# Kernel tuning notes

Hardware: AMD Instinct MI355X
Metric: run time of the kernel (lower is better)

Reference implementation:

```python
import jax, jax.numpy as jnp
import numpy as np

# CondInst DynamicMaskHead dims (defaults from cfg)
N_IMG, C_IN, H, W = 2, 8, 100, 152
N_INST = 500
CHANNELS = 8
STRIDE = 8  # mask_feat_stride (P3)
WEIGHT_NUMS = [(C_IN + 2) * CHANNELS, CHANNELS * CHANNELS, CHANNELS]  # [80, 64, 8]
BIAS_NUMS = [CHANNELS, CHANNELS, 1]
NUM_PARAMS = sum(WEIGHT_NUMS) + sum(BIAS_NUMS)  # 169


def setup_inputs() -> dict:
    key = jax.random.key(0)
    k1, k2, k3, k4, k5 = jax.random.split(key, 5)
    mask_feats = jax.random.normal(k1, (N_IMG, C_IN, H, W), jnp.float32)
    mask_head_params = jax.random.normal(k2, (N_INST, NUM_PARAMS), jnp.float32) * 0.1
    # instance centers in input-image pixel coords
    instance_locations = jax.random.uniform(k3, (N_INST, 2), jnp.float32) * jnp.array([W * STRIDE, H * STRIDE], jnp.float32)
    # sizes_of_interest gathered per instance fpn level (values in [64, 512])
    soi = jax.random.uniform(k4, (N_INST,), jnp.float32) * 448.0 + 64.0
    im_inds = jax.random.randint(k5, (N_INST,), 0, N_IMG)
    return {"mask_feats": mask_feats, "mask_head_params": mask_head_params,
            "instance_locations": instance_locations, "soi": soi, "im_inds": im_inds}


def compute_locations(h, w, stride):
    # matches adet compute_locations: center of each stride cell
    sx = jnp.arange(w, dtype=jnp.float32) * stride + stride // 2
    sy = jnp.arange(h, dtype=jnp.float32) * stride + stride // 2
    gy, gx = jnp.meshgrid(sy, sx, indexing="ij")
    return jnp.stack([gx.ravel(), gy.ravel()], axis=1)  # [H*W, 2] as (x, y)


def parse_dynamic_params(params):
    # faithful to parse_dynamic_params: split weights then biases along dim 1
    sizes = WEIGHT_NUMS + BIAS_NUMS
    splits = jnp.split(params, np.cumsum(sizes)[:-1].tolist(), axis=1)
    w0 = splits[0].reshape(N_INST, CHANNELS, C_IN + 2)   # layer0: (C_in+2)->channels
    w1 = splits[1].reshape(N_INST, CHANNELS, CHANNELS)   # layer1: channels->channels
    w2 = splits[2].reshape(N_INST, 1, CHANNELS)          # layer2: channels->1
    b0, b1, b2 = splits[3], splits[4], splits[5]
    return (w0, w1, w2), (b0, b1, b2)


def reference(mask_feats, mask_head_params, instance_locations, soi, im_inds):
    locations = compute_locations(H, W, STRIDE)  # [HW, 2]
    # relative coords: [n_inst, HW, 2] -> [n_inst, 2, HW], normalized by soi
    rel = (instance_locations[:, None, :] - locations[None, :, :]) / soi[:, None, None]
    rel = jnp.transpose(rel, (0, 2, 1)).astype(mask_feats.dtype)
    feats = mask_feats[im_inds].reshape(N_INST, C_IN, H * W)
    x = jnp.concatenate([rel, feats], axis=1)  # [n_inst, C_in+2, HW]
    (w0, w1, w2), (b0, b1, b2) = parse_dynamic_params(mask_head_params)
    # grouped 1x1 convs (groups=n_inst) == per-instance GEMM over pixels
    x = jax.nn.relu(jnp.einsum("noi,nip->nop", w0, x) + b0[:, :, None])
    x = jax.nn.relu(jnp.einsum("noi,nip->nop", w1, x) + b1[:, :, None])
    x = jnp.einsum("noi,nip->nop", w2, x) + b2[:, :, None]
    return x.reshape(N_INST, 1, H, W)  # mask_logits
```

## Files before the change

kernel.cpp:

```cpp
#include <hip/hip_runtime.h>

#define HGT 100
#define WID 152
#define HW (HGT * WID)
#define NINST 500
#define CIN 8
#define CH 8
#define NPARAMS 169
#define PPT 2


typedef float v2f __attribute__((ext_vector_type(2)));

static __device__ __forceinline__ v2f vsplat2(float x) { v2f r = {x, x}; return r; }

static __device__ __forceinline__ v2f vfma2(float w, v2f x, v2f c) {
#if __has_builtin(__builtin_elementwise_fma)
    return __builtin_elementwise_fma(vsplat2(w), x, c);
#else
    v2f r; r.x = fmaf(w, x.x, c.x); r.y = fmaf(w, x.y, c.y); return r;
#endif
}

static __device__ __forceinline__ v2f vrelu2(v2f a) {
#if __has_builtin(__builtin_elementwise_max)
    return __builtin_elementwise_max(a, vsplat2(0.0f));
#else
    v2f r; r.x = fmaxf(a.x, 0.f); r.y = fmaxf(a.y, 0.f); return r;
#endif
}

__global__ __launch_bounds__(256, 8) void dyn_mask_head(
    const float* __restrict__ feats,
    const float* __restrict__ params,
    const float* __restrict__ locs,
    const float* __restrict__ soi,
    const int*  __restrict__ im_inds,
    float* __restrict__ out)
{
    const int n  = blockIdx.y;
    const int q  = blockIdx.x * blockDim.x + threadIdx.x;
    const int p0 = q * PPT;
    if (p0 >= HW) return;

    const int   im      = im_inds[n];
    const float lx      = locs[n * 2 + 0];
    const float ly      = locs[n * 2 + 1];
    const float inv_soi = 1.0f / soi[n];
    const float* __restrict__ P = params + n * NPARAMS;

    const int py  = p0 / WID;
    const int px0 = p0 - py * WID;
    const float rely = (ly - (float)(py * 8 + 4)) * inv_soi;

    v2f relx;
    relx.x = (lx - (float)(px0 * 8 + 4))  * inv_soi;
    relx.y = (lx - (float)(px0 * 8 + 12)) * inv_soi;

    v2f f[CIN];
    const float* fb = feats + (size_t)im * CIN * HW + p0;
#pragma unroll
    for (int j = 0; j < CIN; ++j) {
        const float2 v = *reinterpret_cast<const float2*>(fb + (size_t)j * HW);
        v2f t = {v.x, v.y};
        f[j] = t;
    }

    v2f h0[CH];
#pragma unroll
    for (int c = 0; c < CH; ++c) {
        const float s = fmaf(P[c * 10 + 1], rely, P[152 + c]);
        v2f acc = vfma2(P[c * 10 + 0], relx, vsplat2(s));
#pragma unroll
        for (int i = 0; i < CIN; ++i)
            acc = vfma2(P[c * 10 + 2 + i], f[i], acc);
        h0[c] = vrelu2(acc);
    }

    v2f h1[CH];
#pragma unroll
    for (int c = 0; c < CH; ++c) {
        v2f acc = vfma2(P[80 + c * 8], h0[0], vsplat2(P[160 + c]));
#pragma unroll
        for (int i = 1; i < CH; ++i)
            acc = vfma2(P[80 + c * 8 + i], h0[i], acc);
        h1[c] = vrelu2(acc);
    }

    v2f o = vfma2(P[144], h1[0], vsplat2(P[168]));
#pragma unroll
    for (int i = 1; i < CH; ++i)
        o = vfma2(P[144 + i], h1[i], o);

    float2 ov; ov.x = o.x; ov.y = o.y;
    *reinterpret_cast<float2*>(out + (size_t)n * HW + p0) = ov;
}

extern "C" void kernel_launch(void* const* d_in, const int* in_sizes, int n_in,
                              void* d_out, int out_size, void* d_ws, size_t ws_size,
                              hipStream_t stream) {
    const float* feats   = (const float*)d_in[0];
    const float* params  = (const float*)d_in[1];
    const float* locs    = (const float*)d_in[2];
    const float* soi     = (const float*)d_in[3];
    const int*   im_inds = (const int*)d_in[4];
    float*       out     = (float*)d_out;

    const int pairs_per_inst = HW / PPT;
    dim3 block(256);
    dim3 grid((pairs_per_inst + block.x - 1) / block.x, NINST);
    dyn_mask_head<<<grid, block, 0, stream>>>(feats, params, locs, soi, im_inds, out);
}
```

Baseline: 35.14 us.

## Rewrite mask head as fp16 MFMA over image-sorted instance quads

Replaces the per-pixel scalar FMA kernel with three kernels. The first sorts instances by image into groups of four, the second prepacks each group's dynamic weights into fp16 MFMA fragments (folding the relative coordinates into an affine hi/lo split), and the third runs 32x32x16 MFMAs per 32-pixel tile across 14 quads per wavefront. It aims to cut the FP32 ALU work and reuse each feature load across many instances. In exchange it adds two extra launches and uses fp16 for weights and activations, which reduces precision.

```diff
diff --git a/kernel.cpp b/kernel.cpp
--- a/kernel.cpp
+++ b/kernel.cpp
@@ -1,99 +1,275 @@
 #include <hip/hip_runtime.h>
+#include <stdint.h>
 
 #define HGT 100
 #define WID 152
 #define HW (HGT * WID)
 #define NINST 500
-#define CIN 8
-#define CH 8
 #define NPARAMS 169
-#define PPT 2
-
-
-typedef float v2f __attribute__((ext_vector_type(2)));
-
-static __device__ __forceinline__ v2f vsplat2(float x) { v2f r = {x, x}; return r; }
-
-static __device__ __forceinline__ v2f vfma2(float w, v2f x, v2f c) {
-#if __has_builtin(__builtin_elementwise_fma)
-    return __builtin_elementwise_fma(vsplat2(w), x, c);
-#else
-    v2f r; r.x = fmaf(w, x.x, c.x); r.y = fmaf(w, x.y, c.y); return r;
-#endif
-}
-
-static __device__ __forceinline__ v2f vrelu2(v2f a) {
-#if __has_builtin(__builtin_elementwise_max)
-    return __builtin_elementwise_max(a, vsplat2(0.0f));
-#else
-    v2f r; r.x = fmaxf(a.x, 0.f); r.y = fmaxf(a.y, 0.f); return r;
-#endif
-}
-
-__global__ __launch_bounds__(256, 8) void dyn_mask_head(
-    const float* __restrict__ feats,
-    const float* __restrict__ params,
-    const float* __restrict__ locs,
-    const float* __restrict__ soi,
-    const int*  __restrict__ im_inds,
+#define NQ 126
+#define QS 12288
+#define FRAG_OFS 4096
+
+typedef __fp16 f16x8  __attribute__((ext_vector_type(8)));
+typedef float  f32x16 __attribute__((ext_vector_type(16)));
+
+static __device__ __forceinline__ uint32_t pkh(float lo, float hi) {
+    __fp16 a = (__fp16)lo, b = (__fp16)hi;
+    uint16_t ua = __builtin_bit_cast(uint16_t, a);
+    uint16_t ub = __builtin_bit_cast(uint16_t, b);
+    return (uint32_t)ua | ((uint32_t)ub << 16);
+}
+
+__global__ __launch_bounds__(512) void sortq(const int* __restrict__ im, int* __restrict__ qtab) {
+    __shared__ int sorted[NINST];
+    __shared__ int wtot0[8], wtot1[8], wex0[8], wex1[8];
+    __shared__ int sc0;
+    const int tid = threadIdx.x;
+    const int lane = tid & 63, w = tid >> 6;
+    const bool valid = tid < NINST;
+    const int img = valid ? im[tid] : -1;
+    const unsigned long long m0 = __ballot(valid && img == 0);
+    const unsigned long long m1 = __ballot(valid && img == 1);
+    const unsigned long long pm = (1ull << lane) - 1ull;
+    const int pre0 = __popcll(m0 & pm);
+    const int pre1 = __popcll(m1 & pm);
+    if (lane == 0) { wtot0[w] = __popcll(m0); wtot1[w] = __popcll(m1); }
+    __syncthreads();
+    if (tid == 0) {
+        int a = 0, b = 0;
+        for (int i = 0; i < 8; ++i) { wex0[i] = a; a += wtot0[i]; wex1[i] = b; b += wtot1[i]; }
+        sc0 = a;
+    }
+    __syncthreads();
+    const int c0 = sc0;
+    if (valid) {
+        const int pos = (img == 0) ? (wex0[w] + pre0) : (c0 + wex1[w] + pre1);
+        sorted[pos] = tid;
+    }
+    __syncthreads();
+    if (tid < NQ) {
+        const int c1 = NINST - c0;
+        const int nq0 = (c0 + 3) >> 2, nq1 = (c1 + 3) >> 2;
+        int i0 = -1, i1 = -1, i2 = -1, i3 = -1, qimg = 0;
+        if (tid < nq0) {
+            qimg = 0;
+            int b = 4 * tid;
+            if (b + 0 < c0) i0 = sorted[b + 0];
+            if (b + 1 < c0) i1 = sorted[b + 1];
+            if (b + 2 < c0) i2 = sorted[b + 2];
+            if (b + 3 < c0) i3 = sorted[b + 3];
+        } else if (tid < nq0 + nq1) {
+            qimg = 1;
+            int b = 4 * (tid - nq0);
+            if (b + 0 < c1) i0 = sorted[c0 + b + 0];
+            if (b + 1 < c1) i1 = sorted[c0 + b + 1];
+            if (b + 2 < c1) i2 = sorted[c0 + b + 2];
+            if (b + 3 < c1) i3 = sorted[c0 + b + 3];
+        }
+        qtab[tid * 5 + 0] = i0; qtab[tid * 5 + 1] = i1;
+        qtab[tid * 5 + 2] = i2; qtab[tid * 5 + 3] = i3;
+        qtab[tid * 5 + 4] = qimg;
+    }
+}
+
+__global__ __launch_bounds__(64) void prepack(
+    const float* __restrict__ params, const float* __restrict__ locs,
+    const float* __restrict__ soi, const int* __restrict__ qtab,
+    uint8_t* __restrict__ frag)
+{
+    const int q = blockIdx.x, l = threadIdx.x;
+    const int id0 = qtab[q * 5 + 0], id1 = qtab[q * 5 + 1];
+    const int id2 = qtab[q * 5 + 2], id3 = qtab[q * 5 + 3];
+    const int qimg = qtab[q * 5 + 4];
+    uint8_t* base = frag + (size_t)q * QS;
+    const int r = l & 31, half = l >> 5, i = r >> 3, c = r & 7;
+    const int n = (i == 0) ? id0 : (i == 1) ? id1 : (i == 2) ? id2 : id3;
+    const bool valid = n >= 0;
+    const float* P = params + (size_t)(valid ? n : 0) * NPARAMS;
+    float lx = 0.f, ly = 0.f, inv = 0.f;
+    if (valid) { lx = locs[2 * n]; ly = locs[2 * n + 1]; inv = 1.0f / soi[n]; }
+    const float wx = valid ? P[c * 10 + 0] : 0.f;
+    const float wy = valid ? P[c * 10 + 1] : 0.f;
+    const float b0 = valid ? P[152 + c] : 0.f;
+    const float Cr = fmaf(wx, (lx - 4.0f) * inv, fmaf(wy, (ly - 4.0f) * inv, b0));
+    const float Ex = -8.0f * wx * inv, Ey = -8.0f * wy * inv;
+    const float Chi = (float)(__fp16)Cr, Clo = Cr - Chi;
+    const float Xhi = (float)(__fp16)Ex, Xlo = Ex - Xhi;
+    const float Yhi = (float)(__fp16)Ey, Ylo = Ey - Yhi;
+    const int jb = half * 8;
+    float v[8];
+#pragma unroll
+    for (int j = 0; j < 8; ++j) {
+        const int k = jb + j;
+        float x;
+        if (k < 8)       x = valid ? P[c * 10 + 2 + k] : 0.f;
+        else if (k == 8)  x = Chi;
+        else if (k == 9)  x = Clo;
+        else if (k == 10) x = Xhi;
+        else if (k == 11) x = Xlo;
+        else if (k == 12) x = Yhi;
+        else if (k == 13) x = Ylo;
+        else              x = 0.f;
+        v[j] = x;
+    }
+    uint4 w0;
+    w0.x = pkh(v[0], v[1]); w0.y = pkh(v[2], v[3]);
+    w0.z = pkh(v[4], v[5]); w0.w = pkh(v[6], v[7]);
+    *reinterpret_cast<uint4*>(base + l * 16) = w0;
+#pragma unroll
+    for (int j = 0; j < 8; ++j) {
+        const int k = jb + j;
+        v[j] = (valid && (k >> 3) == i) ? P[80 + c * 8 + (k & 7)] : 0.f;
+    }
+    uint4 wa;
+    wa.x = pkh(v[0], v[1]); wa.y = pkh(v[2], v[3]);
+    wa.z = pkh(v[4], v[5]); wa.w = pkh(v[6], v[7]);
+    *reinterpret_cast<uint4*>(base + 1024 + l * 16) = wa;
+#pragma unroll
+    for (int j = 0; j < 8; ++j) {
+        const int kk = 16 + jb + j;
+        v[j] = (valid && (kk >> 3) == i) ? P[80 + c * 8 + (kk & 7)] : 0.f;
+    }
+    uint4 wb;
+    wb.x = pkh(v[0], v[1]); wb.y = pkh(v[2], v[3]);
+    wb.z = pkh(v[4], v[5]); wb.w = pkh(v[6], v[7]);
+    *reinterpret_cast<uint4*>(base + 2048 + l * 16) = wb;
+    float bb[16], ww[16];
+#pragma unroll
+    for (int reg = 0; reg < 16; ++reg) {
+        const int ii = reg >> 2;
+        const int cc = (reg & 3) + 4 * half;
+        const int nn = (ii == 0) ? id0 : (ii == 1) ? id1 : (ii == 2) ? id2 : id3;
+        bb[reg] = (nn >= 0) ? params[(size_t)nn * NPARAMS + 160 + cc] : 0.f;
+        ww[reg] = (nn >= 0) ? params[(size_t)nn * NPARAMS + 144 + cc] : 0.f;
+    }
+#pragma unroll
+    for (int j = 0; j < 4; ++j) {
+        float4 tb; tb.x = bb[4 * j]; tb.y = bb[4 * j + 1]; tb.z = bb[4 * j + 2]; tb.w = bb[4 * j + 3];
+        *reinterpret_cast<float4*>(base + 3072 + l * 64 + 16 * j) = tb;
+        float4 tw; tw.x = ww[4 * j]; tw.y = ww[4 * j + 1]; tw.z = ww[4 * j + 2]; tw.w = ww[4 * j + 3];
+        *reinterpret_cast<float4*>(base + 7168 + l * 64 + 16 * j) = tw;
+    }
+    if (l < 4) {
+        const int nn = (l == 0) ? id0 : (l == 1) ? id1 : (l == 2) ? id2 : id3;
+        const uint32_t ofs = (nn >= 0) ? (uint32_t)(nn * HW * 4) : 0xFFFFFFFFu;
+        *reinterpret_cast<uint32_t*>(base + 11264 + l * 4) = ofs;
+        const float b2 = (nn >= 0) ? params[(size_t)nn * NPARAMS + 168] : 0.f;
+        *reinterpret_cast<float*>(base + 11280 + l * 4) = b2;
+    }
+    if (l == 0) *reinterpret_cast<uint32_t*>(base + 11296) = (uint32_t)qimg;
+}
+
+__global__ __launch_bounds__(256) void maskhead(
+    const float* __restrict__ feats, const uint8_t* __restrict__ frag,
     float* __restrict__ out)
 {
-    const int n  = blockIdx.y;
-    const int q  = blockIdx.x * blockDim.x + threadIdx.x;
-    const int p0 = q * PPT;
-    if (p0 >= HW) return;
-
-    const int   im      = im_inds[n];
-    const float lx      = locs[n * 2 + 0];
-    const float ly      = locs[n * 2 + 1];
-    const float inv_soi = 1.0f / soi[n];
-    const float* __restrict__ P = params + n * NPARAMS;
-
-    const int py  = p0 / WID;
-    const int px0 = p0 - py * WID;
-    const float rely = (ly - (float)(py * 8 + 4)) * inv_soi;
-
-    v2f relx;
-    relx.x = (lx - (float)(px0 * 8 + 4))  * inv_soi;
-    relx.y = (lx - (float)(px0 * 8 + 12)) * inv_soi;
-
-    v2f f[CIN];
-    const float* fb = feats + (size_t)im * CIN * HW + p0;
-#pragma unroll
-    for (int j = 0; j < CIN; ++j) {
-        const float2 v = *reinterpret_cast<const float2*>(fb + (size_t)j * HW);
-        v2f t = {v.x, v.y};
-        f[j] = t;
-    }
-
-    v2f h0[CH];
-#pragma unroll
-    for (int c = 0; c < CH; ++c) {
-        const float s = fmaf(P[c * 10 + 1], rely, P[152 + c]);
-        v2f acc = vfma2(P[c * 10 + 0], relx, vsplat2(s));
-#pragma unroll
-        for (int i = 0; i < CIN; ++i)
-            acc = vfma2(P[c * 10 + 2 + i], f[i], acc);
-        h0[c] = vrelu2(acc);
-    }
-
-    v2f h1[CH];
-#pragma unroll
-    for (int c = 0; c < CH; ++c) {
-        v2f acc = vfma2(P[80 + c * 8], h0[0], vsplat2(P[160 + c]));
-#pragma unroll
-        for (int i = 1; i < CH; ++i)
-            acc = vfma2(P[80 + c * 8 + i], h0[i], acc);
-        h1[c] = vrelu2(acc);
-    }
-
-    v2f o = vfma2(P[144], h1[0], vsplat2(P[168]));
-#pragma unroll
-    for (int i = 1; i < CH; ++i)
-        o = vfma2(P[144 + i], h1[i], o);
-
-    float2 ov; ov.x = o.x; ov.y = o.y;
-    *reinterpret_cast<float2*>(out + (size_t)n * HW + p0) = ov;
+    const int wid = threadIdx.x >> 6, lane = threadIdx.x & 63;
+    const int l31 = lane & 31, half = lane >> 5;
+    const int sub = blockIdx.x * 4 + wid;
+    if (sub >= 475) return;
+    const int px = sub * 32 + l31;
+    const int py = px / WID, ux = px - py * WID;
+
+    const uint32_t one2 = 0x3C003C00u;
+    const uint32_t uu = pkh((float)ux, (float)ux);
+    const uint32_t vv = pkh((float)py, (float)py);
+    uint4 t0, t1;
+    if (half == 0) {
+        const float* fb0 = feats + px;
+        const float* fb1 = feats + 8 * HW + px;
+        float f[8], g[8];
+#pragma unroll
+        for (int ch = 0; ch < 8; ++ch) { f[ch] = fb0[(size_t)ch * HW]; g[ch] = fb1[(size_t)ch * HW]; }
+        t0.x = pkh(f[0], f[1]); t0.y = pkh(f[2], f[3]); t0.z = pkh(f[4], f[5]); t0.w = pkh(f[6], f[7]);
+        t1.x = pkh(g[0], g[1]); t1.y = pkh(g[2], g[3]); t1.z = pkh(g[4], g[5]); t1.w = pkh(g[6], g[7]);
+    } else {
+        t0.x = one2; t0.y = uu; t0.z = vv; t0.w = 0u;
+        t1 = t0;
+    }
+    const f16x8 B0a = __builtin_bit_cast(f16x8, t0);
+    const f16x8 B0b = __builtin_bit_cast(f16x8, t1);
+
+    f32x16 z16;
+#pragma unroll
+    for (int e = 0; e < 16; ++e) z16[e] = 0.0f;
+
+    const int qbase = blockIdx.y * 14;
+    for (int t = 0; t < 14; ++t) {
+        const uint8_t* qb = frag + (size_t)(qbase + t) * QS;
+        const uint4 a0w  = *reinterpret_cast<const uint4*>(qb + lane * 16);
+        const uint4 a1aw = *reinterpret_cast<const uint4*>(qb + 1024 + lane * 16);
+        const uint4 a1bw = *reinterpret_cast<const uint4*>(qb + 2048 + lane * 16);
+        const f32x16 bias = *reinterpret_cast<const f32x16*>(qb + 3072 + lane * 64);
+        const f32x16 w2v  = *reinterpret_cast<const f32x16*>(qb + 7168 + lane * 64);
+        const uint4 m0 = *reinterpret_cast<const uint4*>(qb + 11264);
+        const uint4 m1 = *reinterpret_cast<const uint4*>(qb + 11280);
+        const uint32_t mimg = *reinterpret_cast<const uint32_t*>(qb + 11296);
+
+        const f16x8 a0  = __builtin_bit_cast(f16x8, a0w);
+        const f16x8 a1a = __builtin_bit_cast(f16x8, a1aw);
+        const f16x8 a1b = __builtin_bit_cast(f16x8, a1bw);
+        const f16x8 b0  = mimg ? B0b : B0a;
+
+        f32x16 acc0 = __builtin_amdgcn_mfma_f32_32x32x16_f16(a0, b0, z16, 0, 0, 0);
+
+        uint32_t p0, p1, p2, p3, p4, p5, p6, p7;
+        {
+            float lo, hi;
+            lo = fmaxf(acc0[0], 0.f);  hi = fmaxf(acc0[1], 0.f);
+            p0 = __builtin_bit_cast(uint32_t, __builtin_amdgcn_cvt_pkrtz(lo, hi));
+            lo = fmaxf(acc0[2], 0.f);  hi = fmaxf(acc0[3], 0.f);
+            p1 = __builtin_bit_cast(uint32_t, __builtin_amdgcn_cvt_pkrtz(lo, hi));
+            lo = fmaxf(acc0[4], 0.f);  hi = fmaxf(acc0[5], 0.f);
+            p2 = __builtin_bit_cast(uint32_t, __builtin_amdgcn_cvt_pkrtz(lo, hi));
+            lo = fmaxf(acc0[6], 0.f);  hi = fmaxf(acc0[7], 0.f);
+            p3 = __builtin_bit_cast(uint32_t, __builtin_amdgcn_cvt_pkrtz(lo, hi));
+            lo = fmaxf(acc0[8], 0.f);  hi = fmaxf(acc0[9], 0.f);
+            p4 = __builtin_bit_cast(uint32_t, __builtin_amdgcn_cvt_pkrtz(lo, hi));
+            lo = fmaxf(acc0[10], 0.f); hi = fmaxf(acc0[11], 0.f);
+            p5 = __builtin_bit_cast(uint32_t, __builtin_amdgcn_cvt_pkrtz(lo, hi));
+            lo = fmaxf(acc0[12], 0.f); hi = fmaxf(acc0[13], 0.f);
+            p6 = __builtin_bit_cast(uint32_t, __builtin_amdgcn_cvt_pkrtz(lo, hi));
+            lo = fmaxf(acc0[14], 0.f); hi = fmaxf(acc0[15], 0.f);
+            p7 = __builtin_bit_cast(uint32_t, __builtin_amdgcn_cvt_pkrtz(lo, hi));
+        }
+        uint32_t x0 = p0, y0 = p2; asm("v_permlane32_swap_b32 %0, %1" : "+v"(x0), "+v"(y0));
+        uint32_t x1 = p1, y1 = p3; asm("v_permlane32_swap_b32 %0, %1" : "+v"(x1), "+v"(y1));
+        uint32_t x2 = p4, y2 = p6; asm("v_permlane32_swap_b32 %0, %1" : "+v"(x2), "+v"(y2));
+        uint32_t x3 = p5, y3 = p7; asm("v_permlane32_swap_b32 %0, %1" : "+v"(x3), "+v"(y3));
+        uint4 ba; ba.x = x0; ba.y = x1; ba.z = y0; ba.w = y1;
+        uint4 bbv; bbv.x = x2; bbv.y = x3; bbv.z = y2; bbv.w = y3;
+        const f16x8 b1a = __builtin_bit_cast(f16x8, ba);
+        const f16x8 b1b = __builtin_bit_cast(f16x8, bbv);
+
+        f32x16 acc1 = __builtin_amdgcn_mfma_f32_32x32x16_f16(a1a, b1a, bias, 0, 0, 0);
+        acc1 = __builtin_amdgcn_mfma_f32_32x32x16_f16(a1b, b1b, acc1, 0, 0, 0);
+
+        float s0, s1, s2, s3;
+#define L2I(I, SV)                                                                      \
+        {                                                                               \
+            const float h0_ = fmaxf(acc1[4 * I + 0], 0.f);                              \
+            const float h1_ = fmaxf(acc1[4 * I + 1], 0.f);                              \
+            const float h2_ = fmaxf(acc1[4 * I + 2], 0.f);                              \
+            const float h3_ = fmaxf(acc1[4 * I + 3], 0.f);                              \
+            SV = fmaf(w2v[4 * I + 0], h0_, fmaf(w2v[4 * I + 1], h1_,                    \
+                 fmaf(w2v[4 * I + 2], h2_, w2v[4 * I + 3] * h3_)));                     \
+            SV += __shfl_xor(SV, 32);                                                   \
+        }
+        L2I(0, s0) L2I(1, s1) L2I(2, s2) L2I(3, s3)
+#undef L2I
+        s0 += __builtin_bit_cast(float, m1.x);
+        s1 += __builtin_bit_cast(float, m1.y);
+        s2 += __builtin_bit_cast(float, m1.z);
+        s3 += __builtin_bit_cast(float, m1.w);
+
+        if (lane < 32) {
+            if (m0.x != 0xFFFFFFFFu) out[(m0.x >> 2) + px] = s0;
+            if (m0.y != 0xFFFFFFFFu) out[(m0.y >> 2) + px] = s1;
+            if (m0.z != 0xFFFFFFFFu) out[(m0.z >> 2) + px] = s2;
+            if (m0.w != 0xFFFFFFFFu) out[(m0.w >> 2) + px] = s3;
+        }
+    }
 }
 
 extern "C" void kernel_launch(void* const* d_in, const int* in_sizes, int n_in,
@@ -106,8 +282,10 @@
     const int*   im_inds = (const int*)d_in[4];
     float*       out     = (float*)d_out;
 
-    const int pairs_per_inst = HW / PPT;
-    dim3 block(256);
-    dim3 grid((pairs_per_inst + block.x - 1) / block.x, NINST);
-    dyn_mask_head<<<grid, block, 0, stream>>>(feats, params, locs, soi, im_inds, out);
-}
+    int*     qtab = (int*)d_ws;
+    uint8_t* frag = (uint8_t*)d_ws + FRAG_OFS;
+
+    sortq<<<1, 512, 0, stream>>>(im_inds, qtab);
+    prepack<<<NQ, 64, 0, stream>>>(params, locs, soi, qtab, frag);
+    maskhead<<<dim3(119, 9), 256, 0, stream>>>(feats, frag, out);
+}
```

Measured after the change: 60.02 us. 70.8% more time.
